# Kernel tuning notes

Measured on AMD Instinct MI355X. Metric: run time of the kernel, lower is better.

## Reference

```python
import jax, jax.numpy as jnp
import numpy as np

EMB_DIM = 1024
HEAD_DIM = 64
NUM_HEADS = EMB_DIM // HEAD_DIM  # 16
BATCH = 2
SEQ = 2048


def setup_inputs() -> dict:
    key = jax.random.key(0)
    ks = jax.random.split(key, 8)
    s = 0.02
    return {
        "q": jax.random.normal(ks[0], (BATCH, SEQ, EMB_DIM), dtype=jnp.float32),
        "k": jax.random.normal(ks[1], (BATCH, SEQ, EMB_DIM), dtype=jnp.float32),
        "v": jax.random.normal(ks[2], (BATCH, SEQ, EMB_DIM), dtype=jnp.float32),
        "W_q": jax.random.normal(ks[3], (HEAD_DIM, HEAD_DIM), dtype=jnp.float32) * s,
        "W_k": jax.random.normal(ks[4], (HEAD_DIM, HEAD_DIM), dtype=jnp.float32) * s,
        "W_v": jax.random.normal(ks[5], (HEAD_DIM, HEAD_DIM), dtype=jnp.float32) * s,
        "W_fc": jax.random.normal(ks[6], (EMB_DIM, EMB_DIM), dtype=jnp.float32) * s,
        "b_fc": jax.random.normal(ks[7], (EMB_DIM,), dtype=jnp.float32) * s,
    }


def reference(q, k, v, W_q, W_k, W_v, W_fc, b_fc):
    b = v.shape[0]
    # split into heads: [B, S, H, D]
    qh = q.reshape(b, -1, NUM_HEADS, HEAD_DIM)
    kh = k.reshape(b, -1, NUM_HEADS, HEAD_DIM)
    vh = v.reshape(b, -1, NUM_HEADS, HEAD_DIM)
    # per-head shared projections (nn.Linear: x @ W.T, no bias)
    qh = jnp.einsum('bshd,ed->bshe', qh, W_q)
    kh = jnp.einsum('bshd,ed->bshe', kh, W_k)
    vh = jnp.einsum('bshd,ed->bshe', vh, W_v)
    # scores: [B, Q, K, H]
    attn = jnp.einsum('nqhd,nkhd->nqkh', qh, kh)
    # NOTE (faithful to source): softmax over the HEADS axis (dim=3),
    # and scale by sqrt(emb_dim), not sqrt(head_dim).
    attn = jax.nn.softmax(attn / jnp.sqrt(jnp.float32(EMB_DIM)), axis=3)
    # weighted values: [B, Q, H, D] -> [B, Q, EMB]
    out = jnp.einsum('nqkh,nkhd->nqhd', attn, vh).reshape(b, -1, EMB_DIM)
    return out @ W_fc.T + b_fc
```

## Files before the change

kernel.cpp:

```cpp
#include <hip/hip_runtime.h>
#include <hip/hip_bf16.h>

#define S_LEN 2048
#define NHEAD 16
#define HDIM 64
#define EMB 1024

typedef short v8s __attribute__((ext_vector_type(8)));
typedef float v4f __attribute__((ext_vector_type(4)));

__device__ __forceinline__ float bflo(unsigned u) {
    union { unsigned u; float f; } v; v.u = u << 16; return v.f;
}
__device__ __forceinline__ float bfhi(unsigned u) {
    union { unsigned u; float f; } v; v.u = u & 0xFFFF0000u; return v.f;
}
__device__ __forceinline__ unsigned cvtpk(float lo, float hi) {
    union { __hip_bfloat162 h2; unsigned u; } v;
    float2 f; f.x = lo; f.y = hi;
    v.h2 = __float22bfloat162_rn(f);
    return v.u;
}
__device__ __forceinline__ unsigned short f2bf(float f) {
    return (unsigned short)cvtpk(f, f);
}
__device__ __forceinline__ v8s cvt8(float4 a, float4 b) {
    v8s r;
    ((unsigned*)&r)[0] = cvtpk(a.x, a.y);
    ((unsigned*)&r)[1] = cvtpk(a.z, a.w);
    ((unsigned*)&r)[2] = cvtpk(b.x, b.y);
    ((unsigned*)&r)[3] = cvtpk(b.z, b.w);
    return r;
}

__global__ __launch_bounds__(128) void k_proj2(
    const float* __restrict__ q, const float* __restrict__ k, const float* __restrict__ v,
    const float* __restrict__ Wq, const float* __restrict__ Wk, const float* __restrict__ Wv,
    unsigned short* __restrict__ Qp, unsigned short* __restrict__ Kp, unsigned short* __restrict__ Vt)
{
    const int t = threadIdx.x, wave = t >> 6, lane = t & 63;
    const int l15 = lane & 15, l4 = lane >> 4;
    const int mtx = blockIdx.y;
    const int hq = blockIdx.z;
    const int row0 = blockIdx.x * 32 + wave * 16;
    const int b = row0 >> 11, s0 = row0 & 2047;
    const float* X = (mtx == 0) ? q : (mtx == 1) ? k : v;
    const float* W = (mtx == 0) ? Wq : (mtx == 1) ? Wk : Wv;

    v8s wf[4][2];
    #pragma unroll
    for (int tile = 0; tile < 4; ++tile)
        #pragma unroll
        for (int c2 = 0; c2 < 2; ++c2) {
            const float* wp = W + (tile * 16 + l15) * 64 + c2 * 32 + l4 * 8;
            wf[tile][c2] = cvt8(*(const float4*)wp, *(const float4*)(wp + 4));
        }

    #pragma unroll
    for (int hi = 0; hi < 4; ++hi) {
        const int h = hq * 4 + hi;
        v8s xf[2];
        #pragma unroll
        for (int c2 = 0; c2 < 2; ++c2) {
            const float* xp = X + (size_t)(row0 + l15) * EMB + h * 64 + c2 * 32 + l4 * 8;
            xf[c2] = cvt8(*(const float4*)xp, *(const float4*)(xp + 4));
        }
        v4f acc[4];
        #pragma unroll
        for (int i = 0; i < 4; ++i) acc[i] = (v4f){0.f, 0.f, 0.f, 0.f};
        if (mtx < 2) {
            #pragma unroll
            for (int ns = 0; ns < 4; ++ns)
                #pragma unroll
                for (int c2 = 0; c2 < 2; ++c2)
                    acc[ns] = __builtin_amdgcn_mfma_f32_16x16x32_bf16(xf[c2], wf[ns][c2], acc[ns], 0, 0, 0);
            unsigned short* dst = ((mtx == 0) ? Qp : Kp) + (size_t)(b * NHEAD + h) * S_LEN * HDIM;
            #pragma unroll
            for (int ns = 0; ns < 4; ++ns)
                #pragma unroll
                for (int r = 0; r < 4; ++r)
                    dst[(size_t)(s0 + l4 * 4 + r) * HDIM + ns * 16 + l15] = f2bf(acc[ns][r]);
        } else {
            #pragma unroll
            for (int ms = 0; ms < 4; ++ms)
                #pragma unroll
                for (int c2 = 0; c2 < 2; ++c2)
                    acc[ms] = __builtin_amdgcn_mfma_f32_16x16x32_bf16(wf[ms][c2], xf[c2], acc[ms], 0, 0, 0);
            unsigned short* dst = Vt + (size_t)(b * NHEAD + h) * HDIM * S_LEN;
            #pragma unroll
            for (int ms = 0; ms < 4; ++ms)
                #pragma unroll
                for (int r = 0; r < 4; ++r)
                    dst[(size_t)(ms * 16 + l4 * 4 + r) * S_LEN + s0 + l15] = f2bf(acc[ms][r]);
        }
    }
}

__global__ __launch_bounds__(256) void k_cvtw(
    const float* __restrict__ W, unsigned short* __restrict__ Wb)
{
    const int i = (blockIdx.x * 256 + threadIdx.x) * 4;
    float4 wv = *(const float4*)(W + i);
    uint2 pk;
    pk.x = cvtpk(wv.x, wv.y);
    pk.y = cvtpk(wv.z, wv.w);
    *(uint2*)(Wb + i) = pk;
}

__global__ __launch_bounds__(1024, 4) void k_fattn(
    const unsigned short* __restrict__ Qp, const unsigned short* __restrict__ Kp,
    const unsigned short* __restrict__ Vt, unsigned short* __restrict__ Op)
{
    __shared__ unsigned short Pex[16][32][72];
    __shared__ unsigned ZrsU[32][36];
    const int t = threadIdx.x, wave = t >> 6, lane = t & 63;
    const int l15 = lane & 15, l4 = lane >> 4;
    const int h = wave;
    const int id = blockIdx.x;
    const int slot = id & 7;
    const int kqb = slot >> 1;
    const int b = slot & 1;
    const int q0 = (id >> 3) * 32;
    const unsigned short* qh = Qp + (size_t)(b * NHEAD + h) * S_LEN * HDIM;
    const unsigned short* kh = Kp + (size_t)(b * NHEAD + h) * S_LEN * HDIM;
    const unsigned short* vh = Vt + (size_t)(b * NHEAD + h) * HDIM * S_LEN;

    v8s aq[2][2];
    #pragma unroll
    for (int qs = 0; qs < 2; ++qs)
        #pragma unroll
        for (int c2 = 0; c2 < 2; ++c2)
            aq[qs][c2] = *(const v8s*)(qh + (size_t)(q0 + qs * 16 + l15) * HDIM + c2 * 32 + l4 * 8);

    v4f o[2][4];
    #pragma unroll
    for (int qs = 0; qs < 2; ++qs)
        #pragma unroll
        for (int ds = 0; ds < 4; ++ds)
            o[qs][ds] = (v4f){0.f, 0.f, 0.f, 0.f};

    const int zq = t >> 4;
    const int cg = t & 15;

    for (int c = 0; c < 8; ++c) {
        const int kk0 = kqb * 512 + c * 64;
        #pragma unroll
        for (int ks = 0; ks < 4; ++ks) {
            const unsigned short* kb = kh + (size_t)(kk0 + ks * 16 + l15) * HDIM + l4 * 8;
            v8s b0 = *(const v8s*)kb;
            v8s b1 = *(const v8s*)(kb + 32);
            #pragma unroll
            for (int qs = 0; qs < 2; ++qs) {
                v4f sf = (v4f){0.f, 0.f, 0.f, 0.f};
                sf = __builtin_amdgcn_mfma_f32_16x16x32_bf16(aq[qs][0], b0, sf, 0, 0, 0);
                sf = __builtin_amdgcn_mfma_f32_16x16x32_bf16(aq[qs][1], b1, sf, 0, 0, 0);
                const int rb = qs * 16 + l4 * 4;
                unsigned p01 = cvtpk(__expf(sf[0] * 0.03125f), __expf(sf[1] * 0.03125f));
                unsigned p23 = cvtpk(__expf(sf[2] * 0.03125f), __expf(sf[3] * 0.03125f));
                Pex[h][rb + 0][ks * 16 + l15] = (unsigned short)p01;
                Pex[h][rb + 1][ks * 16 + l15] = (unsigned short)(p01 >> 16);
                Pex[h][rb + 2][ks * 16 + l15] = (unsigned short)p23;
                Pex[h][rb + 3][ks * 16 + l15] = (unsigned short)(p23 >> 16);
            }
        }
        __syncthreads();
        if (t < 512) {
            float z0 = 0.f, z1 = 0.f, z2 = 0.f, z3 = 0.f;
            #pragma unroll
            for (int hh = 0; hh < 16; ++hh) {
                uint2 u = *(const uint2*)&Pex[hh][zq][cg * 4];
                z0 += bflo(u.x); z1 += bfhi(u.x);
                z2 += bflo(u.y); z3 += bfhi(u.y);
            }
            uint2 zo;
            zo.x = cvtpk(__builtin_amdgcn_rcpf(z0), __builtin_amdgcn_rcpf(z1));
            zo.y = cvtpk(__builtin_amdgcn_rcpf(z2), __builtin_amdgcn_rcpf(z3));
            *(uint2*)&ZrsU[zq][cg * 2] = zo;
        }
        __syncthreads();
        #pragma unroll
        for (int kp = 0; kp < 2; ++kp) {
            v8s bv[4];
            #pragma unroll
            for (int ds = 0; ds < 4; ++ds)
                bv[ds] = *(const v8s*)(vh + (size_t)(ds * 16 + l15) * S_LEN + kk0 + kp * 32 + l4 * 8);
            #pragma unroll
            for (int qs = 0; qs < 2; ++qs) {
                uint4 pu = *(const uint4*)&Pex[h][qs * 16 + l15][kp * 32 + l4 * 8];
                uint4 zv = *(const uint4*)&ZrsU[qs * 16 + l15][kp * 16 + l4 * 4];
                v8s pn;
                ((unsigned*)&pn)[0] = cvtpk(bflo(pu.x) * bflo(zv.x), bfhi(pu.x) * bfhi(zv.x));
                ((unsigned*)&pn)[1] = cvtpk(bflo(pu.y) * bflo(zv.y), bfhi(pu.y) * bfhi(zv.y));
                ((unsigned*)&pn)[2] = cvtpk(bflo(pu.z) * bflo(zv.z), bfhi(pu.z) * bfhi(zv.z));
                ((unsigned*)&pn)[3] = cvtpk(bflo(pu.w) * bflo(zv.w), bfhi(pu.w) * bfhi(zv.w));
                #pragma unroll
                for (int ds = 0; ds < 4; ++ds)
                    o[qs][ds] = __builtin_amdgcn_mfma_f32_16x16x32_bf16(pn, bv[ds], o[qs][ds], 0, 0, 0);
            }
        }
    }

    unsigned short* op = Op + (size_t)(kqb * 2 + b) * S_LEN * EMB;
    #pragma unroll
    for (int qs = 0; qs < 2; ++qs)
        #pragma unroll
        for (int ds = 0; ds < 4; ++ds)
            #pragma unroll
            for (int r = 0; r < 4; ++r)
                op[(size_t)(q0 + qs * 16 + l4 * 4 + r) * EMB + h * 64 + ds * 16 + l15] =
                    f2bf(o[qs][ds][r]);
}

__global__ __launch_bounds__(256) void k_merge4(
    const unsigned short* __restrict__ Op, unsigned short* __restrict__ AO)
{
    const size_t i = ((size_t)blockIdx.x * 256 + threadIdx.x) * 8;
    const size_t row = i >> 10;
    const int b = (int)(row >> 11);
    const size_t off = (row & 2047) * EMB + (i & 1023);
    float a0 = 0, a1 = 0, a2 = 0, a3 = 0, a4 = 0, a5 = 0, a6 = 0, a7 = 0;
    #pragma unroll
    for (int kq = 0; kq < 4; ++kq) {
        uint4 u = *(const uint4*)(Op + (size_t)(kq * 2 + b) * S_LEN * EMB + off);
        a0 += bflo(u.x); a1 += bfhi(u.x);
        a2 += bflo(u.y); a3 += bfhi(u.y);
        a4 += bflo(u.z); a5 += bfhi(u.z);
        a6 += bflo(u.w); a7 += bfhi(u.w);
    }
    uint4 r;
    r.x = cvtpk(a0, a1); r.y = cvtpk(a2, a3);
    r.z = cvtpk(a4, a5); r.w = cvtpk(a6, a7);
    *(uint4*)(AO + i) = r;
}

__global__ __launch_bounds__(256) void k_fc(
    const unsigned short* __restrict__ AO, const unsigned short* __restrict__ Wb,
    const float* __restrict__ bias, float* __restrict__ out)
{
    const int t = threadIdx.x, wave = t >> 6, lane = t & 63;
    const int l15 = lane & 15, l4 = lane >> 4;
    const int m0 = blockIdx.x * 128 + wave * 32;
    const int n0 = blockIdx.y * 64;
    v4f c[2][4];
    #pragma unroll
    for (int i = 0; i < 2; ++i)
        #pragma unroll
        for (int j = 0; j < 4; ++j) c[i][j] = (v4f){0.f, 0.f, 0.f, 0.f};
    for (int k = 0; k < EMB; k += 32) {
        v8s a0 = *(const v8s*)(AO + (size_t)(m0 + l15) * EMB + k + l4 * 8);
        v8s a1 = *(const v8s*)(AO + (size_t)(m0 + 16 + l15) * EMB + k + l4 * 8);
        #pragma unroll
        for (int ns = 0; ns < 4; ++ns) {
            v8s bw = *(const v8s*)(Wb + (size_t)(n0 + ns * 16 + l15) * EMB + k + l4 * 8);
            c[0][ns] = __builtin_amdgcn_mfma_f32_16x16x32_bf16(a0, bw, c[0][ns], 0, 0, 0);
            c[1][ns] = __builtin_amdgcn_mfma_f32_16x16x32_bf16(a1, bw, c[1][ns], 0, 0, 0);
        }
    }
    #pragma unroll
    for (int ms = 0; ms < 2; ++ms)
        #pragma unroll
        for (int ns = 0; ns < 4; ++ns) {
            const float bv = bias[n0 + ns * 16 + l15];
            #pragma unroll
            for (int r = 0; r < 4; ++r)
                out[(size_t)(m0 + ms * 16 + l4 * 4 + r) * EMB + n0 + ns * 16 + l15] = c[ms][ns][r] + bv;
        }
}

extern "C" void kernel_launch(void* const* d_in, const int* in_sizes, int n_in,
                              void* d_out, int out_size, void* d_ws, size_t ws_size,
                              hipStream_t stream)
{
    (void)in_sizes; (void)n_in; (void)out_size; (void)ws_size;
    const float* q   = (const float*)d_in[0];
    const float* k   = (const float*)d_in[1];
    const float* v   = (const float*)d_in[2];
    const float* Wq  = (const float*)d_in[3];
    const float* Wk  = (const float*)d_in[4];
    const float* Wv  = (const float*)d_in[5];
    const float* Wfc = (const float*)d_in[6];
    const float* bfc = (const float*)d_in[7];

    char* w = (char*)d_ws;
    unsigned short* Qp = (unsigned short*)(w);
    unsigned short* Kp = (unsigned short*)(w + (8u  << 20));
    unsigned short* Vt = (unsigned short*)(w + (16u << 20));
    unsigned short* Wb = (unsigned short*)(w + (24u << 20));
    unsigned short* Op = (unsigned short*)(w + (26u << 20));
    unsigned short* AO = Qp;

    k_proj2 <<<dim3(128, 3, 4), dim3(128),  0, stream>>>(q, k, v, Wq, Wk, Wv, Qp, Kp, Vt);
    k_cvtw  <<<dim3(1024),      dim3(256),  0, stream>>>(Wfc, Wb);
    k_fattn <<<dim3(512),       dim3(1024), 0, stream>>>(Qp, Kp, Vt, Op);
    k_merge4<<<dim3(2048),      dim3(256),  0, stream>>>(Op, AO);
    k_fc    <<<dim3(32, 16),    dim3(256),  0, stream>>>(AO, Wb, bfc, (float*)d_out);
}
```

Measured before the change: 320.5 us.

## Double attention query tile to 64 rows, halve key chunk, stage Q/K stores via LDS

The attention kernel now gives each block 64 query rows instead of 32 and walks keys in 32-wide chunks, halving the grid to 256 blocks. Each K/V fragment loaded from global memory is therefore reused across twice as many query rows, and the normalizer pass uses all 1024 threads. Separately, the Q/K projection output goes through a small LDS tile so it can be written to global memory as coalesced 16-byte stores instead of scattered 2-byte stores. The cost is higher register pressure (more accumulators and Q fragments), twice as many barriers per key range, and fewer blocks to spread over the CUs.

```diff
diff --git a/kernel.cpp b/kernel.cpp
--- a/kernel.cpp
+++ b/kernel.cpp
@@ -38,6 +38,7 @@
     const float* __restrict__ Wq, const float* __restrict__ Wk, const float* __restrict__ Wv,
     unsigned short* __restrict__ Qp, unsigned short* __restrict__ Kp, unsigned short* __restrict__ Vt)
 {
+    __shared__ unsigned short Tq[2][16][72];
     const int t = threadIdx.x, wave = t >> 6, lane = t & 63;
     const int l15 = lane & 15, l4 = lane >> 4;
     const int mtx = blockIdx.y;
@@ -74,12 +75,18 @@
                 #pragma unroll
                 for (int c2 = 0; c2 < 2; ++c2)
                     acc[ns] = __builtin_amdgcn_mfma_f32_16x16x32_bf16(xf[c2], wf[ns][c2], acc[ns], 0, 0, 0);
-            unsigned short* dst = ((mtx == 0) ? Qp : Kp) + (size_t)(b * NHEAD + h) * S_LEN * HDIM;
             #pragma unroll
             for (int ns = 0; ns < 4; ++ns)
                 #pragma unroll
                 for (int r = 0; r < 4; ++r)
-                    dst[(size_t)(s0 + l4 * 4 + r) * HDIM + ns * 16 + l15] = f2bf(acc[ns][r]);
+                    Tq[wave][l4 * 4 + r][ns * 16 + l15] = f2bf(acc[ns][r]);
+            const int row = lane >> 2, c8 = (lane & 3) * 16;
+            uint4 d0 = *(const uint4*)&Tq[wave][row][c8];
+            uint4 d1 = *(const uint4*)&Tq[wave][row][c8 + 8];
+            unsigned short* dst = ((mtx == 0) ? Qp : Kp)
+                + (size_t)(b * NHEAD + h) * S_LEN * HDIM + (size_t)(s0 + row) * HDIM + c8;
+            *(uint4*)dst = d0;
+            *(uint4*)(dst + 8) = d1;
         } else {
             #pragma unroll
             for (int ms = 0; ms < 4; ++ms)
@@ -111,46 +118,48 @@
     const unsigned short* __restrict__ Qp, const unsigned short* __restrict__ Kp,
     const unsigned short* __restrict__ Vt, unsigned short* __restrict__ Op)
 {
-    __shared__ unsigned short Pex[16][32][72];
-    __shared__ unsigned ZrsU[32][36];
+    __shared__ unsigned short Pex[16][64][40];
+    __shared__ unsigned ZrsU[64][20];
     const int t = threadIdx.x, wave = t >> 6, lane = t & 63;
     const int l15 = lane & 15, l4 = lane >> 4;
     const int h = wave;
     const int id = blockIdx.x;
     const int slot = id & 7;
-    const int kqb = slot >> 1;
-    const int b = slot & 1;
-    const int q0 = (id >> 3) * 32;
+    const int kqb = slot & 3;
+    const int bsel = slot >> 2;
+    const int qt = bsel * 32 + (id >> 3);
+    const int b = qt >> 5;
+    const int q0 = (qt & 31) * 64;
     const unsigned short* qh = Qp + (size_t)(b * NHEAD + h) * S_LEN * HDIM;
     const unsigned short* kh = Kp + (size_t)(b * NHEAD + h) * S_LEN * HDIM;
     const unsigned short* vh = Vt + (size_t)(b * NHEAD + h) * HDIM * S_LEN;
 
-    v8s aq[2][2];
-    #pragma unroll
-    for (int qs = 0; qs < 2; ++qs)
+    v8s aq[4][2];
+    #pragma unroll
+    for (int qs = 0; qs < 4; ++qs)
         #pragma unroll
         for (int c2 = 0; c2 < 2; ++c2)
             aq[qs][c2] = *(const v8s*)(qh + (size_t)(q0 + qs * 16 + l15) * HDIM + c2 * 32 + l4 * 8);
 
-    v4f o[2][4];
-    #pragma unroll
-    for (int qs = 0; qs < 2; ++qs)
+    v4f o[4][4];
+    #pragma unroll
+    for (int qs = 0; qs < 4; ++qs)
         #pragma unroll
         for (int ds = 0; ds < 4; ++ds)
             o[qs][ds] = (v4f){0.f, 0.f, 0.f, 0.f};
 
     const int zq = t >> 4;
-    const int cg = t & 15;
-
-    for (int c = 0; c < 8; ++c) {
-        const int kk0 = kqb * 512 + c * 64;
-        #pragma unroll
-        for (int ks = 0; ks < 4; ++ks) {
+    const int zc = t & 15;
+
+    for (int c = 0; c < 16; ++c) {
+        const int kk0 = kqb * 512 + c * 32;
+        #pragma unroll
+        for (int ks = 0; ks < 2; ++ks) {
             const unsigned short* kb = kh + (size_t)(kk0 + ks * 16 + l15) * HDIM + l4 * 8;
             v8s b0 = *(const v8s*)kb;
             v8s b1 = *(const v8s*)(kb + 32);
             #pragma unroll
-            for (int qs = 0; qs < 2; ++qs) {
+            for (int qs = 0; qs < 4; ++qs) {
                 v4f sf = (v4f){0.f, 0.f, 0.f, 0.f};
                 sf = __builtin_amdgcn_mfma_f32_16x16x32_bf16(aq[qs][0], b0, sf, 0, 0, 0);
                 sf = __builtin_amdgcn_mfma_f32_16x16x32_bf16(aq[qs][1], b1, sf, 0, 0, 0);
@@ -164,30 +173,25 @@
             }
         }
         __syncthreads();
-        if (t < 512) {
-            float z0 = 0.f, z1 = 0.f, z2 = 0.f, z3 = 0.f;
+        {
+            float z0 = 0.f, z1 = 0.f;
             #pragma unroll
             for (int hh = 0; hh < 16; ++hh) {
-                uint2 u = *(const uint2*)&Pex[hh][zq][cg * 4];
-                z0 += bflo(u.x); z1 += bfhi(u.x);
-                z2 += bflo(u.y); z3 += bfhi(u.y);
+                unsigned u = *(const unsigned*)&Pex[hh][zq][zc * 2];
+                z0 += bflo(u); z1 += bfhi(u);
             }
-            uint2 zo;
-            zo.x = cvtpk(__builtin_amdgcn_rcpf(z0), __builtin_amdgcn_rcpf(z1));
-            zo.y = cvtpk(__builtin_amdgcn_rcpf(z2), __builtin_amdgcn_rcpf(z3));
-            *(uint2*)&ZrsU[zq][cg * 2] = zo;
+            ZrsU[zq][zc] = cvtpk(__builtin_amdgcn_rcpf(z0), __builtin_amdgcn_rcpf(z1));
         }
         __syncthreads();
-        #pragma unroll
-        for (int kp = 0; kp < 2; ++kp) {
+        {
             v8s bv[4];
             #pragma unroll
             for (int ds = 0; ds < 4; ++ds)
-                bv[ds] = *(const v8s*)(vh + (size_t)(ds * 16 + l15) * S_LEN + kk0 + kp * 32 + l4 * 8);
-            #pragma unroll
-            for (int qs = 0; qs < 2; ++qs) {
-                uint4 pu = *(const uint4*)&Pex[h][qs * 16 + l15][kp * 32 + l4 * 8];
-                uint4 zv = *(const uint4*)&ZrsU[qs * 16 + l15][kp * 16 + l4 * 4];
+                bv[ds] = *(const v8s*)(vh + (size_t)(ds * 16 + l15) * S_LEN + kk0 + l4 * 8);
+            #pragma unroll
+            for (int qs = 0; qs < 4; ++qs) {
+                uint4 pu = *(const uint4*)&Pex[h][qs * 16 + l15][l4 * 8];
+                uint4 zv = *(const uint4*)&ZrsU[qs * 16 + l15][l4 * 4];
                 v8s pn;
                 ((unsigned*)&pn)[0] = cvtpk(bflo(pu.x) * bflo(zv.x), bfhi(pu.x) * bfhi(zv.x));
                 ((unsigned*)&pn)[1] = cvtpk(bflo(pu.y) * bflo(zv.y), bfhi(pu.y) * bfhi(zv.y));
@@ -202,7 +206,7 @@
 
     unsigned short* op = Op + (size_t)(kqb * 2 + b) * S_LEN * EMB;
     #pragma unroll
-    for (int qs = 0; qs < 2; ++qs)
+    for (int qs = 0; qs < 4; ++qs)
         #pragma unroll
         for (int ds = 0; ds < 4; ++ds)
             #pragma unroll
@@ -291,7 +295,7 @@
 
     k_proj2 <<<dim3(128, 3, 4), dim3(128),  0, stream>>>(q, k, v, Wq, Wk, Wv, Qp, Kp, Vt);
     k_cvtw  <<<dim3(1024),      dim3(256),  0, stream>>>(Wfc, Wb);
-    k_fattn <<<dim3(512),       dim3(1024), 0, stream>>>(Qp, Kp, Vt, Op);
+    k_fattn <<<dim3(256),       dim3(1024), 0, stream>>>(Qp, Kp, Vt, Op);
     k_merge4<<<dim3(2048),      dim3(256),  0, stream>>>(Op, AO);
     k_fc    <<<dim3(32, 16),    dim3(256),  0, stream>>>(AO, Wb, bfc, (float*)d_out);
 }
```

New measurement: 277.7 us. -13.3%, faster.
